# Performance work log

Measured on AMD Instinct MI355X. Metric: run time of the kernel, lower is better.

Reference implementation:

```python
import jax, jax.numpy as jnp
import numpy as np

EPS = 1e-4
TAU = 0.1
GAMMA = 64.0
RADIUS = 1.0
N_HEADS = 4
N_SPLIT = 4


def _l2norm(x, axis=-1):
    return x / jnp.maximum(jnp.linalg.norm(x, axis=axis, keepdims=True), 1e-12)


def _pd2(a, b):
    # pairwise squared distances: (B,N,M)
    return (jnp.sum(a * a, -1)[:, :, None] + jnp.sum(b * b, -1)[:, None, :]
            - 2.0 * jnp.einsum('bnd,bmd->bnm', a, b))


def _sim_matrix(xyz, nf, radius, gamma):
    # radius-masked Gaussian feature affinity, zero diagonal
    N = xyz.shape[1]
    d2x = _pd2(xyz, xyz)
    d2f = _pd2(nf, nf)
    A = jnp.exp(-gamma * d2f / nf.shape[-1]) * (d2x < radius * radius).astype(nf.dtype)
    return A * (1.0 - jnp.eye(N, dtype=A.dtype))


def _norm_lap(A, eps):
    deg = A.sum(-1)
    dinv = jax.lax.rsqrt(deg + eps)
    na = A * dinv[:, :, None] * dinv[:, None, :]
    lap = jnp.eye(A.shape[1], dtype=A.dtype) - na
    return lap, na


def _mincut(X, na, W1, b1, W2, b2, tau):
    # one GCN layer + temperature softmax soft assignment; pooled = weighted mean
    h = jax.nn.relu(jnp.einsum('bnm,bmc->bnc', na, X) @ W1 + b1)
    s = jax.nn.softmax((h @ W2 + b2) / tau, axis=-1)  # (B,N,K)
    denom = s.sum(1)[:, :, None] + EPS                # (B,K,1)
    c_fea = jnp.einsum('bnk,bnc->bkc', s, X) / denom
    return c_fea, s


def _centers(xyz, s):
    denom = s.sum(1)[:, :, None] + EPS
    return jnp.einsum('bnk,bnd->bkd', s, xyz) / denom


def _assignment_loss(p_xyz, c_xyz, s):
    d2 = _pd2(p_xyz, c_xyz)
    return jnp.mean(jnp.sum(s * d2, -1))


def _welsch(p_xyz, c_xyz, sigma):
    d2min = jnp.min(_pd2(p_xyz, c_xyz), -1)
    return jnp.mean(1.0 - jnp.exp(-d2min / (2.0 * sigma * sigma)))


def _knn_affinity(xyz, k):
    N = xyz.shape[1]
    d2 = _pd2(xyz, xyz)
    eye = jnp.eye(N, dtype=d2.dtype)
    neg = -(d2 + 1e6 * eye)
    thresh = jax.lax.top_k(neg, k)[0][..., -1:]
    mask = (neg >= thresh).astype(d2.dtype)
    A = jnp.exp(-d2) * mask * (1.0 - eye)
    return jnp.maximum(A, jnp.swapaxes(A, 1, 2))


def _cut_loss(na, xyz, alpha):
    N = xyz.shape[1]
    lap = jnp.eye(N, dtype=na.dtype) - na
    quad = jnp.einsum('bnd,bnm,bmd->b', xyz, lap, xyz)
    return alpha * jnp.mean(quad / N)


def _cross_attn(gf, cf, Wq, Wk, Wv, Wo, n_heads):
    B, N, C = gf.shape
    M = cf.shape[1]
    dh = C // n_heads
    q = (gf @ Wq).reshape(B, N, n_heads, dh)
    k = (cf @ Wk).reshape(B, M, n_heads, dh)
    v = (cf @ Wv).reshape(B, M, n_heads, dh)
    scores = jnp.einsum('bnhd,bmhd->bhnm', q, k) / np.sqrt(dh).astype(np.float32)
    attn = jax.nn.softmax(scores, -1)
    out = jnp.einsum('bhnm,bmhd->bnhd', attn, v).reshape(B, N, C) @ Wo
    return out, attn.mean(1)


def setup_inputs() -> dict:
    key = jax.random.key(0)
    ks = jax.random.split(key, 20)
    B, N_sp, C, H, K = 2, 1024, 256, 128, 64
    Kg = K // N_SPLIT
    sc = 1.0 / np.sqrt(C)
    sh = 1.0 / np.sqrt(H)
    return {
        'g_fea': jax.random.normal(ks[0], (B, N_sp, C), jnp.float32),
        'g_xyz': jax.random.uniform(ks[1], (B, N_sp, 3), jnp.float32),
        'p_fea_0': jax.random.normal(ks[2], (B, 4096, C), jnp.float32),
        'p_xyz_0': jax.random.uniform(ks[3], (B, 4096, 3), jnp.float32),
        'p_fea_1': jax.random.normal(ks[4], (B, 2048, C), jnp.float32),
        'p_xyz_1': jax.random.uniform(ks[5], (B, 2048, 3), jnp.float32),
        'lW1': jax.random.normal(ks[6], (C, H), jnp.float32) * sc,
        'lb1': jnp.zeros((H,), jnp.float32),
        'lW2': jax.random.normal(ks[7], (H, K), jnp.float32) * sh,
        'lb2': jnp.zeros((K,), jnp.float32),
        'gW1': jax.random.normal(ks[8], (C, H), jnp.float32) * sc,
        'gb1': jnp.zeros((H,), jnp.float32),
        'gW2': jax.random.normal(ks[9], (H, Kg), jnp.float32) * sh,
        'gb2': jnp.zeros((Kg,), jnp.float32),
        'Wq': jax.random.normal(ks[10], (C, C), jnp.float32) * sc,
        'Wk': jax.random.normal(ks[11], (C, C), jnp.float32) * sc,
        'Wv': jax.random.normal(ks[12], (C, C), jnp.float32) * sc,
        'Wo': jax.random.normal(ks[13], (C, C), jnp.float32) * sc,
    }


def reference(g_fea, g_xyz, p_fea_0, p_xyz_0, p_fea_1, p_xyz_1,
              lW1, lb1, lW2, lb2, gW1, gb1, gW2, gb2, Wq, Wk, Wv, Wo):
    l_loss = jnp.zeros((), jnp.float32)
    cx_list, cf_list = [], []
    for p_xyz_i, p_fea_i in ((p_xyz_0, p_fea_0), (p_xyz_1, p_fea_1)):
        nf = _l2norm(p_fea_i)
        A = _sim_matrix(p_xyz_i, nf, RADIUS, GAMMA)
        na = _norm_lap(A, EPS)[1]
        c_fea_i, s_i = _mincut(p_fea_i, na, lW1, lb1, lW2, lb2, TAU)
        c_xyz_i = _centers(p_xyz_i, s_i)
        c2p = jnp.einsum('bnk,bkc->bnc', s_i, jax.lax.stop_gradient(c_fea_i))
        l_loss = l_loss + _assignment_loss(p_xyz_i, c_xyz_i, s_i)
        l_loss = l_loss + jnp.linalg.norm(_l2norm(c2p) - nf) + _welsch(p_xyz_i, c_xyz_i, 1.0)
        cx_list.append(c_xyz_i)
        cf_list.append(c_fea_i)
    c_xyz = jnp.concatenate(cx_list, 1)
    c_fea = jnp.concatenate(cf_list, 1)
    A_c = _knn_affinity(c_xyz, 2 * N_SPLIT)
    na_c = _norm_lap(A_c, EPS)[1]
    c_fea_g, gs = _mincut(c_fea, na_c, gW1, gb1, gW2, gb2, TAU)
    c_xyz_g = _centers(c_xyz, gs)
    cut_loss_c = _assignment_loss(c_xyz, c_xyz_g, gs)
    agg, G_t = _cross_attn(g_fea, c_fea_g, Wq, Wk, Wv, Wo, N_HEADS)
    A_g = _sim_matrix(g_xyz, _l2norm(g_fea), 4.0 * RADIUS, GAMMA)
    ass_loss = _cut_loss(_norm_lap(A_g, EPS)[1], g_xyz, 1e-4)
    g_loss = jnp.mean(jnp.sum(jnp.linalg.norm(_l2norm(agg) - _l2norm(g_fea), axis=-1), 1)) + ass_loss
    return agg, l_loss + cut_loss_c, g_loss
```

## Files before the change

kernel.cpp:

```cpp
#include <hip/hip_runtime.h>

#define EPSF 1e-4f

typedef __attribute__((ext_vector_type(8))) short bf16x8;
typedef __attribute__((ext_vector_type(4))) float f32x4;

__device__ __forceinline__ unsigned short f2bf(float f){
    unsigned int u = __float_as_uint(f);
    return (unsigned short)((u + 0x7FFF + ((u >> 16) & 1)) >> 16);
}
__device__ __forceinline__ float bf2f(unsigned short u){
    return __uint_as_float(((unsigned int)u) << 16);
}
__device__ __forceinline__ float waveSum(float v){
    #pragma unroll
    for (int o = 32; o; o >>= 1) v += __shfl_xor(v, o, 64);
    return v;
}
__device__ __forceinline__ float waveMin(float v){
    #pragma unroll
    for (int o = 32; o; o >>= 1) v = fminf(v, __shfl_xor(v, o, 64));
    return v;
}
__device__ __forceinline__ float waveMax(float v){
// ... 5 lines not shown
    int t = threadIdx.x;
    red[t] = v; __syncthreads();
    for (int s = nthr >> 1; s > 0; s >>= 1){
        if (t < s) red[t] += red[t + s];
        __syncthreads();
    }
    float r = red[0]; __syncthreads();
    return r;
}

__global__ void l2norm_kernel(const float* __restrict__ x, float* __restrict__ outf,
                              unsigned short* __restrict__ outb, int rows){
    __shared__ float red[256];
    int row = blockIdx.x, t = threadIdx.x;
    float v = x[(long)row*256 + t];
    float s = blockReduceSum(v*v, red, 256);
    float nrm = fmaxf(sqrtf(s), 1e-12f);
    float r = v / nrm;
    outf[(long)row*256 + t] = r;
    outb[(long)row*256 + t] = f2bf(r);
}

__global__ void cvt_bf16_kernel(const float* __restrict__ in, unsigned short* __restrict__ out, long n4){
    long i = (long)blockIdx.x*256 + threadIdx.x;
    if (i < n4){
        float4 v = ((const float4*)in)[i];
        unsigned int lo = f2bf(v.x) | ((unsigned int)f2bf(v.y) << 16);
        unsigned int hi = f2bf(v.z) | ((unsigned int)f2bf(v.w) << 16);
        uint2 u; u.x = lo; u.y = hi;
        ((uint2*)out)[i] = u;
    }
}

__global__ void tcvt_kernel(const float* __restrict__ W, unsigned short* __restrict__ WT,
                            int Rw, int Cw){
    __shared__ float tile[64][65];
    int r0 = blockIdx.x*64, c0 = blockIdx.y*64;
    int t = threadIdx.x;
    for (int idx = t; idx < 4096; idx += 256){
        int rr = idx >> 6, cc = idx & 63;
        tile[rr][cc] = (r0+rr < Rw && c0+cc < Cw) ? W[(long)(r0+rr)*Cw + c0+cc] : 0.f;
    }
    __syncthreads();
    for (int idx = t; idx < 4096; idx += 256){
        int cc = idx >> 6, rr = idx & 63;
        if (r0+rr < Rw && c0+cc < Cw)
            WT[(long)(c0+cc)*Rw + r0+rr] = f2bf(tile[rr][cc]);
    }
}

__global__ __launch_bounds__(256) void gram_mfma_kernel(const unsigned short* __restrict__ nf,
                                                        const float* __restrict__ xyz,
                                                        unsigned short* __restrict__ A,
                                                        int N, float r2, float scale){
    __shared__ short tA[128*32], tB[128*32];
    __shared__ float xa[384], xb[384];
    int tid = threadIdx.x;
    int n0 = blockIdx.y*128, m0 = blockIdx.x*128;
    for (int i = tid; i < 384; i += 256){ xa[i] = xyz[n0*3 + i]; xb[i] = xyz[m0*3 + i]; }
    int w = tid >> 6, l = tid & 63;
    int wy = w >> 1, wx = w & 1;
    int lg = l >> 4, lr = l & 15;
    int srow = tid >> 2, sc = tid & 3;
    f32x4 zero = {0.f, 0.f, 0.f, 0.f};
    f32x4 acc[4][4];
    #pragma unroll
    for (int i = 0; i < 4; ++i)
        #pragma unroll
        for (int j = 0; j < 4; ++j) acc[i][j] = zero;
    for (int kt = 0; kt < 256; kt += 32){
        __syncthreads();
        #pragma unroll
        for (int p = 0; p < 2; ++p){
            int row = srow + p*64;
            uint4 va = *(const uint4*)(nf + (long)(n0+row)*256 + kt + sc*8);
            uint4 vb = *(const uint4*)(nf + (long)(m0+row)*256 + kt + sc*8);
            *(uint4*)(tA + row*32 + sc*8) = va;
            *(uint4*)(tB + row*32 + sc*8) = vb;
        }
        __syncthreads();
        bf16x8 af[4], bfr[4];
        #pragma unroll
        for (int f = 0; f < 4; ++f){
            af[f]  = *(const bf16x8*)(tA + (wy*64 + f*16 + lr)*32 + lg*8);
            bfr[f] = *(const bf16x8*)(tB + (wx*64 + f*16 + lr)*32 + lg*8);
        }
        #pragma unroll
        for (int i = 0; i < 4; ++i)
            #pragma unroll
            for (int j = 0; j < 4; ++j)
                acc[i][j] = __builtin_amdgcn_mfma_f32_16x16x32_bf16(af[i], bfr[j], acc[i][j], 0, 0, 0);
    }
    #pragma unroll
    for (int fi = 0; fi < 4; ++fi){
        #pragma unroll
        for (int fj = 0; fj < 4; ++fj){
            #pragma unroll
            for (int r = 0; r < 4; ++r){
                int n_ = wy*64 + fi*16 + lg*4 + r;
                int m_ = wx*64 + fj*16 + lr;
                float dx = xa[n_*3+0]-xb[m_*3+0];
                float dy = xa[n_*3+1]-xb[m_*3+1];
                float dz = xa[n_*3+2]-xb[m_*3+2];
                float d2x = dx*dx + dy*dy + dz*dz;
                int gn = n0 + n_, gm = m0 + m_;
                float dot = acc[fi][fj][r];
                float val = (d2x < r2 && gn != gm) ? expf(scale*(2.f*dot - 2.f)) : 0.f;
                A[(long)gn*N + gm] = f2bf(val);
            }
        }
    }
}

__global__ void rowsum_kernel(const unsigned short* __restrict__ A, float* __restrict__ dinv, int N){
    __shared__ float red[256];
    int n = blockIdx.x, t = threadIdx.x;
    const uint4* row = (const uint4*)(A + (long)n*N);
    float s = 0.f;
    for (int i = t; i < N/8; i += 256){
        uint4 u = row[i];
        s += __uint_as_float(u.x << 16) + __uint_as_float(u.x & 0xFFFF0000u);
        s += __uint_as_float(u.y << 16) + __uint_as_float(u.y & 0xFFFF0000u);
        s += __uint_as_float(u.z << 16) + __uint_as_float(u.z & 0xFFFF0000u);
        s += __uint_as_float(u.w << 16) + __uint_as_float(u.w & 0xFFFF0000u);
    }
    s = blockReduceSum(s, red, 256);
    if (t == 0) dinv[n] = rsqrtf(s + EPSF);
}

__global__ __launch_bounds__(256) void transpose_scale_kernel(const float* __restrict__ fea,
                                                              const float* __restrict__ dinv,
                                                              unsigned short* __restrict__ feaT,
                                                              unsigned short* __restrict__ xsT, int N){
    __shared__ float tile[64][65];
    __shared__ float dl[64];
    int m0 = blockIdx.x*64, c0 = blockIdx.y*64;
    int t = threadIdx.x;
    int lr = t >> 2, lc = (t & 3)*16;
    #pragma unroll
    for (int j = 0; j < 4; ++j){
        float4 v = *(const float4*)(fea + (long)(m0+lr)*256 + c0 + lc + j*4);
        tile[lr][lc+j*4+0] = v.x; tile[lr][lc+j*4+1] = v.y;
        tile[lr][lc+j*4+2] = v.z; tile[lr][lc+j*4+3] = v.w;
    }
    if (t < 64) dl[t] = dinv[m0+t];
    __syncthreads();
    unsigned short vr[16] __attribute__((aligned(16)));
    unsigned short vs[16] __attribute__((aligned(16)));
    #pragma unroll
    for (int j = 0; j < 16; ++j){
        float raw = tile[lc+j][lr];
        vr[j] = f2bf(raw);
        vs[j] = f2bf(raw * dl[lc+j]);
    }
    long off = (long)(c0+lr)*N + m0 + lc;
    *(uint4*)(feaT + off)     = *(uint4*)&vr[0];
    *(uint4*)(feaT + off + 8) = *(uint4*)&vr[8];
    *(uint4*)(xsT + off)      = *(uint4*)&vs[0];
    *(uint4*)(xsT + off + 8)  = *(uint4*)&vs[8];
}

__global__ __launch_bounds__(256) void ax_mfma_kernel(const unsigned short* __restrict__ A,
                                                      const unsigned short* __restrict__ xsT,
                                                      float* __restrict__ PY, int N){
    __shared__ short tA[128*32], tB[128*32];
    int tid = threadIdx.x;
    int c0 = blockIdx.x*128, n0 = blockIdx.y*128;
    int half = blockIdx.z;
    int kbase = half*(N/2), kend = kbase + N/2;
    int w = tid >> 6, l = tid & 63;
    int wy = w >> 1, wx = w & 1;
    int lg = l >> 4, lr = l & 15;
    int srow = tid >> 2, sc = tid & 3;
    f32x4 zero = {0.f, 0.f, 0.f, 0.f};
    f32x4 acc[4][4];
    #pragma unroll
    for (int i = 0; i < 4; ++i)
        #pragma unroll
        for (int j = 0; j < 4; ++j) acc[i][j] = zero;
    for (int kt = kbase; kt < kend; kt += 32){
        __syncthreads();
        #pragma unroll
        for (int p = 0; p < 2; ++p){
            int row = srow + p*64;
            uint4 va = *(const uint4*)(A   + (long)(n0+row)*N + kt + sc*8);
            uint4 vb = *(const uint4*)(xsT + (long)(c0+row)*N + kt + sc*8);
            *(uint4*)(tA + row*32 + sc*8) = va;
            *(uint4*)(tB + row*32 + sc*8) = vb;
        }
        __syncthreads();
        bf16x8 af[4], bfr[4];
        #pragma unroll
        for (int f = 0; f < 4; ++f){
            af[f]  = *(const bf16x8*)(tA + (wy*64 + f*16 + lr)*32 + lg*8);
            bfr[f] = *(const bf16x8*)(tB + (wx*64 + f*16 + lr)*32 + lg*8);
        }
        #pragma unroll
        for (int i = 0; i < 4; ++i)
            #pragma unroll
            for (int j = 0; j < 4; ++j)
                acc[i][j] = __builtin_amdgcn_mfma_f32_16x16x32_bf16(af[i], bfr[j], acc[i][j], 0, 0, 0);
    }
    float* out = PY + (long)half*N*256;
    #pragma unroll
    for (int fi = 0; fi < 4; ++fi){
        #pragma unroll
        for (int fj = 0; fj < 4; ++fj){
            #pragma unroll
            for (int r = 0; r < 4; ++r){
                int n_ = n0 + wy*64 + fi*16 + lg*4 + r;
                int c_ = c0 + wx*64 + fj*16 + lr;
                out[(long)n_*256 + c_] = acc[fi][fj][r];
            }
        }
    }
}

__global__ void combine_kernel(const float* __restrict__ PY, const float* __restrict__ dinv,
                               unsigned short* __restrict__ Yb, int N){
    long i = (long)blockIdx.x*256 + threadIdx.x;
    long e = i*8;
    const float4* p0 = (const float4*)(PY + e);
    const float4* p1 = (const float4*)(PY + (long)N*256 + e);
    float4 a0 = p0[0], a1 = p0[1], b0 = p1[0], b1 = p1[1];
    float d = dinv[e >> 8];
    unsigned short vb[8] __attribute__((aligned(16)));
    vb[0] = f2bf((a0.x+b0.x)*d); vb[1] = f2bf((a0.y+b0.y)*d);
    vb[2] = f2bf((a0.z+b0.z)*d); vb[3] = f2bf((a0.w+b0.w)*d);
    vb[4] = f2bf((a1.x+b1.x)*d); vb[5] = f2bf((a1.y+b1.y)*d);
    vb[6] = f2bf((a1.z+b1.z)*d); vb[7] = f2bf((a1.w+b1.w)*d);
    *(uint4*)(Yb + e) = *(uint4*)vb;
}

__global__ __launch_bounds__(256) void gemm_XW_mfma_kernel(const unsigned short* __restrict__ X,
                                                           const unsigned short* __restrict__ WT,
                                                           const float* __restrict__ bias,
                                                           float* __restrict__ outF,
                                                           unsigned short* __restrict__ outB,
                                                           int R, int Ci, int Co, int relu){
    __shared__ short tA[128*32], tB[128*32];
    int tid = threadIdx.x;
    int c0 = blockIdx.x*128, r0 = blockIdx.y*128;
    int w = tid >> 6, l = tid & 63;
    int wy = w >> 1, wx = w & 1;
    int lg = l >> 4, lr = l & 15;
    int srow = tid >> 2, sc = tid & 3;
    f32x4 zero = {0.f, 0.f, 0.f, 0.f};
    f32x4 acc[4][4];
    #pragma unroll
    for (int i = 0; i < 4; ++i)
        #pragma unroll
        for (int j = 0; j < 4; ++j) acc[i][j] = zero;
    for (int kt = 0; kt < Ci; kt += 32){
        __syncthreads();
        #pragma unroll
        for (int p = 0; p < 2; ++p){
            int row = srow + p*64;
            uint4 va = {0,0,0,0}, vb = {0,0,0,0};
            int ar = r0 + row, br = c0 + row;
            if (ar < R)  va = *(const uint4*)(X  + (long)ar*Ci + kt + sc*8);
            if (br < Co) vb = *(const uint4*)(WT + (long)br*Ci + kt + sc*8);
            *(uint4*)(tA + row*32 + sc*8) = va;
            *(uint4*)(tB + row*32 + sc*8) = vb;
        }
        __syncthreads();
        bf16x8 af[4], bfr[4];
        #pragma unroll
        for (int f = 0; f < 4; ++f){
            af[f]  = *(const bf16x8*)(tA + (wy*64 + f*16 + lr)*32 + lg*8);
            bfr[f] = *(const bf16x8*)(tB + (wx*64 + f*16 + lr)*32 + lg*8);
        }
        #pragma unroll
        for (int i = 0; i < 4; ++i)
            #pragma unroll
            for (int j = 0; j < 4; ++j)
                acc[i][j] = __builtin_amdgcn_mfma_f32_16x16x32_bf16(af[i], bfr[j], acc[i][j], 0, 0, 0);
    }
    #pragma unroll
    for (int fi = 0; fi < 4; ++fi){
        #pragma unroll
        for (int fj = 0; fj < 4; ++fj){
            #pragma unroll
            for (int r = 0; r < 4; ++r){
                int rr = r0 + wy*64 + fi*16 + lg*4 + r;
                int cc = c0 + wx*64 + fj*16 + lr;
                if (rr < R && cc < Co){
                    float v = acc[fi][fj][r] + (bias ? bias[cc] : 0.f);
                    if (relu) v = fmaxf(v, 0.f);
                    if (outF) outF[(long)rr*Co + cc] = v;
                    if (outB) outB[(long)rr*Co + cc] = f2bf(v);
                }
            }
        }
    }
}

__global__ __launch_bounds__(256) void softmaxT_kernel(float* __restrict__ s,
                                                       unsigned short* __restrict__ sT,
                                                       int sStride, float invtau){
    __shared__ unsigned short st[64][65];
    int blk = blockIdx.x, t = threadIdx.x, w = t >> 6, l = t & 63;
    #pragma unroll
    for (int i = 0; i < 16; ++i){
        int rloc = w + 4*i;
        long row = (long)blk*64 + rloc;
        float v = s[row*64 + l] * invtau;
        float mx = waveMax(v);
        float e = expf(v - mx);
        float sum = waveSum(e);
        float p = e / sum;
        s[row*64 + l] = p;
        st[l][rloc] = f2bf(p);
    }
    __syncthreads();
    int k = t >> 2, j = (t & 3)*16;
    unsigned short vbuf[16] __attribute__((aligned(16)));
    #pragma unroll
    for (int q = 0; q < 16; ++q) vbuf[q] = st[k][j+q];
    long off = (long)k*sStride + (long)blk*64 + j;
    *(uint4*)(sT + off)     = *(uint4*)&vbuf[0];
    *(uint4*)(sT + off + 8) = *(uint4*)&vbuf[8];
}

__global__ __launch_bounds__(256) void stx_mfma_kernel(const unsigned short* __restrict__ sT,
                                                       const unsigned short* __restrict__ feaT,
                                                       float* __restrict__ part,
                                                       int N, int split, int sStride){
    __shared__ short tA[64*32], tB[256*32];
    int tid = threadIdx.x;
    int z = blockIdx.x, b = z / split, chunk = z % split;
    int L = N / split, kst = chunk * L;
    const unsigned short* sTb = sT + (long)b*N;
    const unsigned short* fT  = feaT + (long)b*256*N;
    int w = tid >> 6, l = tid & 63;
    int lg = l >> 4, lr = l & 15;
    f32x4 zero = {0.f, 0.f, 0.f, 0.f};
    f32x4 acc[4][4];
    #pragma unroll
    for (int i = 0; i < 4; ++i)
        #pragma unroll
        for (int j = 0; j < 4; ++j) acc[i][j] = zero;
    int srow = tid >> 2, koff = (tid & 3)*8;
    for (int kt = kst; kt < kst + L; kt += 32){
        __syncthreads();
        *(uint4*)(tA + srow*32 + koff) = *(const uint4*)(sTb + (long)srow*sStride + kt + koff);
        #pragma unroll
        for (int p = 0; p < 4; ++p){
            int row = srow + p*64;
            *(uint4*)(tB + row*32 + koff) = *(const uint4*)(fT + (long)row*N + kt + koff);
        }
        __syncthreads();
        bf16x8 af[4], bfr[4];
        #pragma unroll
        for (int f = 0; f < 4; ++f){
            af[f]  = *(const bf16x8*)(tA + (f*16 + lr)*32 + lg*8);
            bfr[f] = *(const bf16x8*)(tB + (w*64 + f*16 + lr)*32 + lg*8);
        }
        #pragma unroll
        for (int i = 0; i < 4; ++i)
            #pragma unroll
            for (int j = 0; j < 4; ++j)
                acc[i][j] = __builtin_amdgcn_mfma_f32_16x16x32_bf16(af[i], bfr[j], acc[i][j], 0, 0, 0);
    }
    float* outp = part + (long)z*64*256;
    #pragma unroll
    for (int fi = 0; fi < 4; ++fi){
        #pragma unroll
        for (int fj = 0; fj < 4; ++fj){
            #pragma unroll
            for (int r = 0; r < 4; ++r){
                int kc = fi*16 + lg*4 + r;
                int cc = w*64 + fj*16 + lr;
                outp[(long)kc*256 + cc] = acc[fi][fj][r];
            }
        }
    }
}

__global__ __launch_bounds__(256) void gemm_XW_kernel(const float* __restrict__ X,
                                                      const float* __restrict__ W,
                                                      const float* __restrict__ bias,
                                                      float* __restrict__ out,
                                                      int R, int Ci, int Co, int relu){
    __shared__ float sa[32][65], sb[32][65];
    int tid = threadIdx.x, tx = tid & 15, ty = tid >> 4;
    int c0 = blockIdx.x * 64, r0 = blockIdx.y * 64;
    float acc[4][4] = {};
    for (int kt = 0; kt < Ci; kt += 32){
        #pragma unroll
        for (int p = 0; p < 8; ++p){
            int idx = p*256 + tid;
            int k = idx & 31, i = idx >> 5;
            int rr = r0 + i;
            sa[k][i] = (rr < R) ? X[(long)rr*Ci + kt + k] : 0.f;
            int j = idx & 63, kk = idx >> 6;
            int cc = c0 + j;
            sb[kk][j] = (cc < Co) ? W[(long)(kt+kk)*Co + cc] : 0.f;
        }
        __syncthreads();
        #pragma unroll
        for (int k = 0; k < 32; ++k){
            float a0=sa[k][ty*4+0],a1=sa[k][ty*4+1],a2=sa[k][ty*4+2],a3=sa[k][ty*4+3];
            float b0=sb[k][tx*4+0],b1=sb[k][tx*4+1],b2=sb[k][tx*4+2],b3=sb[k][tx*4+3];
            acc[0][0]+=a0*b0; acc[0][1]+=a0*b1; acc[0][2]+=a0*b2; acc[0][3]+=a0*b3;
            acc[1][0]+=a1*b0; acc[1][1]+=a1*b1; acc[1][2]+=a1*b2; acc[1][3]+=a1*b3;
            acc[2][0]+=a2*b0; acc[2][1]+=a2*b1; acc[2][2]+=a2*b2; acc[2][3]+=a2*b3;
            acc[3][0]+=a3*b0; acc[3][1]+=a3*b1; acc[3][2]+=a3*b2; acc[3][3]+=a3*b3;
        }
        __syncthreads();
    }
    #pragma unroll
    for (int r = 0; r < 4; ++r){
        #pragma unroll
        for (int c = 0; c < 4; ++c){
            int rr = r0 + ty*4 + r, cc = c0 + tx*4 + c;
            if (rr < R && cc < Co){
                float v = acc[r][c] + (bias ? bias[cc] : 0.f);
                if (relu) v = fmaxf(v, 0.f);
                out[(long)rr*Co + cc] = v;
            }
        }
    }
}

__global__ void softmax_kernel(float* __restrict__ x, int Kc, float tau){
    int row = blockIdx.x, lane = threadIdx.x;
    bool act = lane < Kc;
    float v = act ? x[(long)row*Kc + lane] / tau : -1e30f;
    float mx = v;
    #pragma unroll
    for (int o = 32; o; o >>= 1) mx = fmaxf(mx, __shfl_xor(mx, o, 64));
    float e = act ? expf(v - mx) : 0.f;
    float s = e;
    #pragma unroll
    for (int o = 32; o; o >>= 1) s += __shfl_xor(s, o, 64);
    if (act) x[(long)row*Kc + lane] = e / s;
}

__global__ void cluster_xyz_kernel(const float* __restrict__ s, const float* __restrict__ xyz,
                                   float* __restrict__ outx, float* __restrict__ outd,
                                   int N, int Kc, int xBS, int dBS){
    __shared__ float red[256];
    int b = blockIdx.y, k = blockIdx.x, t = threadIdx.x;
    s   += (long)b*N*Kc;
    xyz += (long)b*N*3;
    float a0=0,a1=0,a2=0,ad=0;
    for (int n = t; n < N; n += 256){
        float sv = s[(long)n*Kc + k];
        ad += sv;
        a0 += sv*xyz[n*3+0]; a1 += sv*xyz[n*3+1]; a2 += sv*xyz[n*3+2];
    }
    a0 = blockReduceSum(a0, red, 256);
    a1 = blockReduceSum(a1, red, 256);
    a2 = blockReduceSum(a2, red, 256);
    ad = blockReduceSum(ad, red, 256);
    if (t == 0){
        outx[b*xBS + k*3+0] = a0;
        outx[b*xBS + k*3+1] = a1;
        outx[b*xBS + k*3+2] = a2;
        outd[b*dBS + k] = ad;
    }
}

__global__ __launch_bounds__(256) void gemm_sTX_kernel(const float* __restrict__ s,
                                                       const float* __restrict__ X,
                                                       float* __restrict__ part,
                                                       int N, int Kc, int split,
                                                       long sBS, long xBS){
    __shared__ float sa[32][65], sb[32][65];
    int tid = threadIdx.x, tx = tid & 15, ty = tid >> 4;
    int c0 = blockIdx.x * 64;
    int b = blockIdx.z / split, chunk = blockIdx.z % split;
// ... 153 lines not shown

__global__ void cutc_kernel(const float* __restrict__ gs, const float* __restrict__ cxyz,
                            const float* __restrict__ cxyzg, float* __restrict__ scal, float inv){
    __shared__ float cg[48];
    __shared__ float red[128];
    int b = blockIdx.x, t = threadIdx.x;
    if (t < 48) cg[t] = cxyzg[b*48 + t];
    __syncthreads();
    float x0 = cxyz[b*384 + t*3+0], x1 = cxyz[b*384 + t*3+1], x2 = cxyz[b*384 + t*3+2];
    float acc = 0.f;
    #pragma unroll
    for (int k = 0; k < 16; ++k){
        float dx = x0-cg[k*3+0], dy = x1-cg[k*3+1], dz = x2-cg[k*3+2];
        acc += gs[b*2048 + t*16 + k]*(dx*dx+dy*dy+dz*dz);
    }
    acc = blockReduceSum(acc, red, 128);
    if (t == 0) atomicAdd(&scal[b], acc*inv);
}

__global__ __launch_bounds__(256) void attn_kernel(const float* __restrict__ q,
                                                   const float* __restrict__ kk,
                                                   const float* __restrict__ vv,
                                                   unsigned short* __restrict__ aob){
    __shared__ float Ks[16][256], Vs[16][256];
    int b = blockIdx.y, n = blockIdx.x, t = threadIdx.x;
    #pragma unroll
    for (int p = 0; p < 16; ++p){
        int j = p*256 + t;
        Ks[j>>8][j&255] = kk[b*4096 + j];
        Vs[j>>8][j&255] = vv[b*4096 + j];
    }
    __syncthreads();
    float qv = q[((long)b*1024 + n)*256 + t];
    float sc[16];
    #pragma unroll
    for (int m = 0; m < 16; ++m){
        float v = qv * Ks[m][t];
        #pragma unroll
        for (int o = 32; o; o >>= 1) v += __shfl_xor(v, o, 64);
        sc[m] = v * 0.125f;
    }
    float mx = -1e30f;
    #pragma unroll
    for (int m = 0; m < 16; ++m) mx = fmaxf(mx, sc[m]);
    float sum = 0.f;
    #pragma unroll
    for (int m = 0; m < 16; ++m){ sc[m] = expf(sc[m]-mx); sum += sc[m]; }
    float o = 0.f;
    #pragma unroll
    for (int m = 0; m < 16; ++m) o += sc[m]*Vs[m][t];
    aob[((long)b*1024 + n)*256 + t] = f2bf(o / sum);
}

__global__ void quad_kernel(const unsigned short* __restrict__ A, const float* __restrict__ dinv,
                            const float* __restrict__ xyz, float* __restrict__ scal){
    __shared__ float part[4];
    int t = threadIdx.x, w = t >> 6, l = t & 63;
    int n = blockIdx.x*4 + w;
    float a0=0,a1=0,a2=0;
    #pragma unroll 4
    for (int i = 0; i < 16; ++i){
        int m = l + i*64;
        float wv = bf2f(A[(long)n*1024 + m])*dinv[m];
        a0 += wv*xyz[m*3+0]; a1 += wv*xyz[m*3+1]; a2 += wv*xyz[m*3+2];
    }
    a0 = waveSum(a0); a1 = waveSum(a1); a2 = waveSum(a2);
    if (l == 0){
        float x0 = xyz[n*3+0], x1 = xyz[n*3+1], x2 = xyz[n*3+2];
        part[w] = (x0*x0+x1*x1+x2*x2) - dinv[n]*(x0*a0+x1*a1+x2*a2);
    }
    __syncthreads();
    if (t == 0) atomicAdd(&scal[4*64 + (blockIdx.x & 63)], part[0]+part[1]+part[2]+part[3]);
}

__global__ void gloss_kernel(const float* __restrict__ agg, const float* __restrict__ gfea,
                             float* __restrict__ scal){
    __shared__ float part[4];
    int t = threadIdx.x, w = t >> 6, l = t & 63;
    long r = (long)blockIdx.x*4 + w;
    const float* a = agg + r*256;
    const float* g = gfea + r*256;
    float a0=a[l],a1=a[l+64],a2=a[l+128],a3=a[l+192];
    float g0=g[l],g1=g[l+64],g2=g[l+128],g3=g[l+192];
    float na2 = waveSum(a0*a0+a1*a1+a2*a2+a3*a3);
    float ng2 = waveSum(g0*g0+g1*g1+g2*g2+g3*g3);
    float ia = 1.f/fmaxf(sqrtf(na2), 1e-12f), ig = 1.f/fmaxf(sqrtf(ng2), 1e-12f);
    float e0=a0*ia-g0*ig, e1=a1*ia-g1*ig, e2=a2*ia-g2*ig, e3=a3*ia-g3*ig;
    float d2 = waveSum(e0*e0+e1*e1+e2*e2+e3*e3);
    if (l == 0) part[w] = sqrtf(d2);
    __syncthreads();
    if (t == 0) atomicAdd(&scal[3*64 + (blockIdx.x & 63)], part[0]+part[1]+part[2]+part[3]);
}

__global__ void finalize_kernel(const float* __restrict__ scal, float* __restrict__ out){
    int t = threadIdx.x;
    float s[5];
    #pragma unroll
    for (int q = 0; q < 5; ++q){
        float v = scal[q*64 + t];
        #pragma unroll
        for (int o = 32; o; o >>= 1) v += __shfl_xor(v, o, 64);
        s[q] = v;
    }
    if (t == 0){
        out[524288] = s[0] + sqrtf(s[1]) + sqrtf(s[2]);
        out[524289] = s[3]*0.5f + 1e-4f*s[4]/2048.0f;
    }
}

extern "C" void kernel_launch(void* const* d_in, const int* in_sizes, int n_in,
                              void* d_out, int out_size, void* d_ws, size_t ws_size,
                              hipStream_t stream){
    const float* g_fea   = (const float*)d_in[0];
    const float* g_xyz   = (const float*)d_in[1];
    const float* p_fea_0 = (const float*)d_in[2];
    const float* p_xyz_0 = (const float*)d_in[3];
    const float* p_fea_1 = (const float*)d_in[4];
    const float* p_xyz_1 = (const float*)d_in[5];
    const float* lW1 = (const float*)d_in[6];
    const float* lb1 = (const float*)d_in[7];
    const float* lW2 = (const float*)d_in[8];
    const float* lb2 = (const float*)d_in[9];
    const float* gW1 = (const float*)d_in[10];
    const float* gb1 = (const float*)d_in[11];
    const float* gW2 = (const float*)d_in[12];
    const float* gb2 = (const float*)d_in[13];
    const float* Wq = (const float*)d_in[14];
    const float* Wk = (const float*)d_in[15];
    const float* Wv = (const float*)d_in[16];
    const float* Wo = (const float*)d_in[17];
    float* out = (float*)d_out;
    float* ws_f = (float*)d_ws;

    constexpr long O_SCALS = 0;
    constexpr long O_CFEA  = 512;
    constexpr long O_CXYZ  = O_CFEA + 65536;
    constexpr long O_DEN   = O_CXYZ + 768;
    constexpr long O_CFG   = O_DEN  + 256;
    constexpr long O_CXG   = O_CFG  + 8192;
    constexpr long O_DENG  = O_CXG  + 96;
    constexpr long O_PART  = O_DENG + 64;
    constexpr long O_NF    = O_PART + 262144;
    constexpr long O_NFB   = O_NF   + 2097152;
    constexpr long O_XST   = O_NFB  + 1048576;
    constexpr long O_FEAT  = O_XST  + 1048576;
    constexpr long O_YB    = O_FEAT + 1048576;
    constexpr long O_HB    = O_YB   + 1048576;
    constexpr long O_S     = O_HB   + 524288;
    constexpr long O_ST    = O_S    + 524288;
    constexpr long O_DINV  = O_ST   + 262144;
    constexpr long O_PY    = O_DINV + 8192;
    constexpr long O_A     = O_PY   + 2097152;
    constexpr long O_Q     = O_A    + 8388608;
    constexpr long O_GFB   = O_Q    + 524288;
    constexpr long O_AOB   = O_GFB  + 262144;
    constexpr long O_KK    = O_AOB  + 262144;
    constexpr long O_VV    = O_KK   + 8192;
    constexpr long O_NAC   = O_VV   + 8192;
    constexpr long O_Y2    = O_NAC  + 32768;
    constexpr long O_H2    = O_Y2   + 65536;
    constexpr long O_LG2   = O_H2   + 32768;
    constexpr long O_W1T   = O_LG2  + 4096;
    constexpr long O_W2T   = O_W1T  + 16384;
    constexpr long O_WQT   = O_W2T  + 4096;
    constexpr long O_WOT   = O_WQT  + 32768;

    hipMemsetAsync(ws_f + O_SCALS, 0, 512*sizeof(float), stream);

    float* nf   = ws_f + O_NF;
    unsigned short* nfb  = (unsigned short*)(ws_f + O_NFB);
    unsigned short* xsT  = (unsigned short*)(ws_f + O_XST);
    unsigned short* feaT = (unsigned short*)(ws_f + O_FEAT);
    unsigned short* Ybb  = (unsigned short*)(ws_f + O_YB);
    unsigned short* Hb   = (unsigned short*)(ws_f + O_HB);
    unsigned short* sTb  = (unsigned short*)(ws_f + O_ST);
    unsigned short* A    = (unsigned short*)(ws_f + O_A);
    unsigned short* gfb  = (unsigned short*)(ws_f + O_GFB);
    unsigned short* aob  = (unsigned short*)(ws_f + O_AOB);
    unsigned short* lW1T = (unsigned short*)(ws_f + O_W1T);
    unsigned short* lW2T = (unsigned short*)(ws_f + O_W2T);
    unsigned short* WqT  = (unsigned short*)(ws_f + O_WQT);
    unsigned short* WoT  = (unsigned short*)(ws_f + O_WOT);
    float* sb   = ws_f + O_S;
    float* dinv = ws_f + O_DINV;
    float* PY   = ws_f + O_PY;
    float* part = ws_f + O_PART;
    float* Qf   = ws_f + O_Q;

    tcvt_kernel<<<dim3(4, 2), 256, 0, stream>>>(lW1, lW1T, 256, 128);
    tcvt_kernel<<<dim3(2, 1), 256, 0, stream>>>(lW2, lW2T, 128, 64);
    tcvt_kernel<<<dim3(4, 4), 256, 0, stream>>>(Wq, WqT, 256, 256);
    tcvt_kernel<<<dim3(4, 4), 256, 0, stream>>>(Wo, WoT, 256, 256);
    cvt_bf16_kernel<<<512, 256, 0, stream>>>(g_fea, gfb, 131072);

    struct Lvl { const float* fea; const float* xyz; int N; int k0; int ndsSlot; };
    Lvl lv[2] = {{p_fea_0, p_xyz_0, 4096, 0, 1}, {p_fea_1, p_xyz_1, 2048, 64, 2}};

    for (int L = 0; L < 2; ++L){
        int N = lv[L].N;
        const float* fea = lv[L].fea;
        const float* xyz = lv[L].xyz;
        l2norm_kernel<<<2*N, 256, 0, stream>>>(fea, nf, nfb, 2*N);
        for (int b = 0; b < 2; ++b){
            const unsigned short* nfbb = nfb + (long)b*N*256;
            const float* xyzb = xyz + (long)b*N*3;
            gram_mfma_kernel<<<dim3(N/128, N/128), 256, 0, stream>>>(nfbb, xyzb, A, N, 1.0f, 0.25f);
            rowsum_kernel<<<N, 256, 0, stream>>>(A, dinv + b*N, N);
            transpose_scale_kernel<<<dim3(N/64, 4), 256, 0, stream>>>(fea + (long)b*N*256, dinv + b*N,
                                                                      feaT + (long)b*256*N,
                                                                      xsT + (long)b*256*N, N);
            ax_mfma_kernel<<<dim3(2, N/128, 2), 256, 0, stream>>>(A, xsT + (long)b*256*N, PY, N);
            combine_kernel<<<N/8, 256, 0, stream>>>(PY, dinv + b*N, Ybb + (long)b*N*256, N);
        }
        gemm_XW_mfma_kernel<<<dim3(1, 2*N/128), 256, 0, stream>>>(Ybb, lW1T, lb1, nullptr, Hb,
                                                                  2*N, 256, 128, 1);
        gemm_XW_mfma_kernel<<<dim3(1, 2*N/128), 256, 0, stream>>>(Hb, lW2T, lb2, sb, nullptr,
                                                                  2*N, 128, 64, 0);
        softmaxT_kernel<<<2*N/64, 256, 0, stream>>>(sb, sTb, 2*N, 10.0f);
        cluster_xyz_kernel<<<dim3(64, 2), 256, 0, stream>>>(sb, xyz, ws_f + O_CXYZ + lv[L].k0*3,
                                                            ws_f + O_DEN + lv[L].k0, N, 64, 384, 128);
        stx_mfma_kernel<<<16, 256, 0, stream>>>(sTb, feaT, part, N, 8, 2*N);
        divide_sum_kernel<<<dim3(64, 2), 256, 0, stream>>>(part, ws_f + O_DEN + lv[L].k0,
                                                           ws_f + O_CFEA + lv[L].k0*256,
                                                           ws_f + O_CXYZ + lv[L].k0*3,
                                                           64, 8, 128*256, 384, 128);
        level_loss_kernel<<<dim3(N/4, 2), 256, 0, stream>>>(sb, xyz, ws_f + O_CXYZ + lv[L].k0*3,
                                                            ws_f + O_CFEA + lv[L].k0*256, nf,
                                                            ws_f + O_SCALS, N, 1.0f/(2.0f*N), lv[L].ndsSlot);
    }

    knn_nac_kernel<<<2, 128, 0, stream>>>(ws_f + O_CXYZ, ws_f + O_NAC);
    bmm_small_kernel<<<dim3(128, 2), 256, 0, stream>>>(ws_f + O_NAC, ws_f + O_CFEA, ws_f + O_Y2);
    gemm_XW_kernel<<<dim3(2, 4), 256, 0, stream>>>(ws_f + O_Y2, gW1, gb1, ws_f + O_H2, 256, 256, 128, 1);
    gemm_XW_kernel<<<dim3(1, 4), 256, 0, stream>>>(ws_f + O_H2, gW2, gb2, ws_f + O_LG2, 256, 128, 16, 0);
    softmax_kernel<<<256, 64, 0, stream>>>(ws_f + O_LG2, 16, 0.1f);
    cluster_xyz_kernel<<<dim3(16, 2), 256, 0, stream>>>(ws_f + O_LG2, ws_f + O_CXYZ,
                                                        ws_f + O_CXG, ws_f + O_DENG, 128, 16, 48, 16);
    gemm_sTX_kernel<<<dim3(4, 1, 2), 256, 0, stream>>>(ws_f + O_LG2, ws_f + O_CFEA, part,
                                                       128, 16, 1, 128L*16, 128L*256);
    divide_sum_kernel<<<dim3(16, 2), 256, 0, stream>>>(part, ws_f + O_DENG, ws_f + O_CFG,
                                                       ws_f + O_CXG, 16, 1, 16*256, 48, 16);
    cutc_kernel<<<2, 128, 0, stream>>>(ws_f + O_LG2, ws_f + O_CXYZ, ws_f + O_CXG,
                                       ws_f + O_SCALS, 1.0f/256.0f);

    gemm_XW_mfma_kernel<<<dim3(2, 16), 256, 0, stream>>>(gfb, WqT, nullptr, Qf, nullptr,
                                                         2048, 256, 256, 0);
    gemm_XW_kernel<<<dim3(4, 1), 256, 0, stream>>>(ws_f + O_CFG, Wk, nullptr, ws_f + O_KK, 32, 256, 256, 0);
    gemm_XW_kernel<<<dim3(4, 1), 256, 0, stream>>>(ws_f + O_CFG, Wv, nullptr, ws_f + O_VV, 32, 256, 256, 0);
    attn_kernel<<<dim3(1024, 2), 256, 0, stream>>>(Qf, ws_f + O_KK, ws_f + O_VV, aob);
    gemm_XW_mfma_kernel<<<dim3(2, 16), 256, 0, stream>>>(aob, WoT, nullptr, out, nullptr,
                                                         2048, 256, 256, 0);

    l2norm_kernel<<<2048, 256, 0, stream>>>(g_fea, nf, nfb, 2048);
    for (int b = 0; b < 2; ++b){
        gram_mfma_kernel<<<dim3(8, 8), 256, 0, stream>>>(nfb + (long)b*1024*256, g_xyz + (long)b*1024*3,
                                                         A, 1024, 16.0f, 0.25f);
        rowsum_kernel<<<1024, 256, 0, stream>>>(A, dinv + b*1024, 1024);
        quad_kernel<<<256, 256, 0, stream>>>(A, dinv + b*1024, g_xyz + (long)b*1024*3, ws_f + O_SCALS);
    }

    gloss_kernel<<<512, 256, 0, stream>>>(out, g_fea, ws_f + O_SCALS);
    finalize_kernel<<<1, 64, 0, stream>>>(ws_f + O_SCALS, out);
}
```

Measured before the change: 906.8 us.

## Fuse degree rowsum into gram epilogue and split-K the small GEMMs

The gram kernel now accumulates each row's affinity sum in its epilogue, reduces it across lanes, and atomically adds it into a zeroed degree buffer. This removes the separate rowsum kernel, which re-read the whole bf16 affinity matrix, and consumers compute rsqrt(deg+eps) themselves. The small FP32 GEMMs on the global level and for K/V are replaced by a split-K kernel plus a combine kernel, and the stx and sTX reductions use more splits, to raise parallelism on tiny problems. The cost is atomics, extra combine launches, a larger workspace memset, and degrees summed in fp32 before bf16 rounding, which differs slightly from summing the rounded bf16 values.

```diff
diff --git a/kernel.cpp b/kernel.cpp
--- a/kernel.cpp
+++ b/kernel.cpp
@@ -81,6 +81,7 @@
 __global__ __launch_bounds__(256) void gram_mfma_kernel(const unsigned short* __restrict__ nf,
                                                         const float* __restrict__ xyz,
                                                         unsigned short* __restrict__ A,
+                                                        float* __restrict__ deg,
                                                         int N, float r2, float scale){
     __shared__ short tA[128*32], tB[128*32];
     __shared__ float xa[384], xb[384];
@@ -123,42 +124,34 @@
     #pragma unroll
     for (int fi = 0; fi < 4; ++fi){
         #pragma unroll
-        for (int fj = 0; fj < 4; ++fj){
+        for (int r = 0; r < 4; ++r){
+            int n_ = wy*64 + fi*16 + lg*4 + r;
+            int gn = n0 + n_;
+            float rowacc = 0.f;
             #pragma unroll
-            for (int r = 0; r < 4; ++r){
-                int n_ = wy*64 + fi*16 + lg*4 + r;
+            for (int fj = 0; fj < 4; ++fj){
                 int m_ = wx*64 + fj*16 + lr;
                 float dx = xa[n_*3+0]-xb[m_*3+0];
                 float dy = xa[n_*3+1]-xb[m_*3+1];
                 float dz = xa[n_*3+2]-xb[m_*3+2];
                 float d2x = dx*dx + dy*dy + dz*dz;
-                int gn = n0 + n_, gm = m0 + m_;
+                int gm = m0 + m_;
                 float dot = acc[fi][fj][r];
                 float val = (d2x < r2 && gn != gm) ? expf(scale*(2.f*dot - 2.f)) : 0.f;
                 A[(long)gn*N + gm] = f2bf(val);
+                rowacc += val;
             }
-        }
-    }
-}
-
-__global__ void rowsum_kernel(const unsigned short* __restrict__ A, float* __restrict__ dinv, int N){
-    __shared__ float red[256];
-    int n = blockIdx.x, t = threadIdx.x;
-    const uint4* row = (const uint4*)(A + (long)n*N);
-    float s = 0.f;
-    for (int i = t; i < N/8; i += 256){
-        uint4 u = row[i];
-        s += __uint_as_float(u.x << 16) + __uint_as_float(u.x & 0xFFFF0000u);
-        s += __uint_as_float(u.y << 16) + __uint_as_float(u.y & 0xFFFF0000u);
-        s += __uint_as_float(u.z << 16) + __uint_as_float(u.z & 0xFFFF0000u);
-        s += __uint_as_float(u.w << 16) + __uint_as_float(u.w & 0xFFFF0000u);
-    }
-    s = blockReduceSum(s, red, 256);
-    if (t == 0) dinv[n] = rsqrtf(s + EPSF);
+            rowacc += __shfl_xor(rowacc, 1, 64);
+            rowacc += __shfl_xor(rowacc, 2, 64);
+            rowacc += __shfl_xor(rowacc, 4, 64);
+            rowacc += __shfl_xor(rowacc, 8, 64);
+            if (lr == 0) atomicAdd(&deg[gn], rowacc);
+        }
+    }
 }
 
 __global__ __launch_bounds__(256) void transpose_scale_kernel(const float* __restrict__ fea,
-                                                              const float* __restrict__ dinv,
+                                                              const float* __restrict__ deg,
                                                               unsigned short* __restrict__ feaT,
                                                               unsigned short* __restrict__ xsT, int N){
     __shared__ float tile[64][65];
@@ -172,7 +165,7 @@
         tile[lr][lc+j*4+0] = v.x; tile[lr][lc+j*4+1] = v.y;
         tile[lr][lc+j*4+2] = v.z; tile[lr][lc+j*4+3] = v.w;
     }
-    if (t < 64) dl[t] = dinv[m0+t];
+    if (t < 64) dl[t] = rsqrtf(deg[m0+t] + EPSF);
     __syncthreads();
     unsigned short vr[16] __attribute__((aligned(16)));
     unsigned short vs[16] __attribute__((aligned(16)));
@@ -245,14 +238,14 @@
     }
 }
 
-__global__ void combine_kernel(const float* __restrict__ PY, const float* __restrict__ dinv,
+__global__ void combine_kernel(const float* __restrict__ PY, const float* __restrict__ deg,
                                unsigned short* __restrict__ Yb, int N){
     long i = (long)blockIdx.x*256 + threadIdx.x;
     long e = i*8;
     const float4* p0 = (const float4*)(PY + e);
     const float4* p1 = (const float4*)(PY + (long)N*256 + e);
     float4 a0 = p0[0], a1 = p0[1], b0 = p1[0], b1 = p1[1];
-    float d = dinv[e >> 8];
+    float d = rsqrtf(deg[e >> 8] + EPSF);
     unsigned short vb[8] __attribute__((aligned(16)));
     vb[0] = f2bf((a0.x+b0.x)*d); vb[1] = f2bf((a0.y+b0.y)*d);
     vb[2] = f2bf((a0.z+b0.z)*d); vb[3] = f2bf((a0.w+b0.w)*d);
@@ -324,6 +317,65 @@
     }
 }
 
+__global__ __launch_bounds__(256) void gemm_splitk_kernel(const float* __restrict__ X,
+                                                          const float* __restrict__ W0,
+                                                          const float* __restrict__ W1,
+                                                          float* __restrict__ part,
+                                                          int R, int Ci, int Co, int Ks){
+    __shared__ float sa[32][65], sb[32][65];
+    int tid = threadIdx.x, tx = tid & 15, ty = tid >> 4;
+    int c0 = blockIdx.x * 64, r0 = blockIdx.y * 64;
+    int z = blockIdx.z;
+    const float* W = (z / Ks) ? W1 : W0;
+    int kchunk = Ci / Ks, kst = (z % Ks) * kchunk;
+    float acc[4][4] = {};
+    for (int kt = kst; kt < kst + kchunk; kt += 32){
+        #pragma unroll
+        for (int p = 0; p < 8; ++p){
+            int idx = p*256 + tid;
+            int k = idx & 31, i = idx >> 5;
+            int rr = r0 + i;
+            sa[k][i] = (rr < R) ? X[(long)rr*Ci + kt + k] : 0.f;
+            int j = idx & 63, kk = idx >> 6;
+            int cc = c0 + j;
+            sb[kk][j] = (cc < Co) ? W[(long)(kt+kk)*Co + cc] : 0.f;
+        }
+        __syncthreads();
+        #pragma unroll
+        for (int k = 0; k < 32; ++k){
+            float a0=sa[k][ty*4+0],a1=sa[k][ty*4+1],a2=sa[k][ty*4+2],a3=sa[k][ty*4+3];
+            float b0=sb[k][tx*4+0],b1=sb[k][tx*4+1],b2=sb[k][tx*4+2],b3=sb[k][tx*4+3];
+            acc[0][0]+=a0*b0; acc[0][1]+=a0*b1; acc[0][2]+=a0*b2; acc[0][3]+=a0*b3;
+            acc[1][0]+=a1*b0; acc[1][1]+=a1*b1; acc[1][2]+=a1*b2; acc[1][3]+=a1*b3;
+            acc[2][0]+=a2*b0; acc[2][1]+=a2*b1; acc[2][2]+=a2*b2; acc[2][3]+=a2*b3;
+            acc[3][0]+=a3*b0; acc[3][1]+=a3*b1; acc[3][2]+=a3*b2; acc[3][3]+=a3*b3;
+        }
+        __syncthreads();
+    }
+    float* outp = part + (long)z*R*Co;
+    #pragma unroll
+    for (int r = 0; r < 4; ++r){
+        #pragma unroll
+        for (int c = 0; c < 4; ++c){
+            int rr = r0 + ty*4 + r, cc = c0 + tx*4 + c;
+            if (rr < R && cc < Co) outp[(long)rr*Co + cc] = acc[r][c];
+        }
+    }
+}
+
+__global__ void combine_bias_kernel(const float* __restrict__ part, const float* __restrict__ bias,
+                                    float* __restrict__ out, int R, int Co, int Ks, int relu){
+    long i = (long)blockIdx.x*256 + threadIdx.x;
+    if (i < (long)R*Co){
+        long zs = (long)R*Co;
+        float s = 0.f;
+        for (int q = 0; q < Ks; ++q) s += part[q*zs + i];
+        float v = s + (bias ? bias[i % Co] : 0.f);
+        if (relu) v = fmaxf(v, 0.f);
+        out[i] = v;
+    }
+}
+
 __global__ __launch_bounds__(256) void softmaxT_kernel(float* __restrict__ s,
                                                        unsigned short* __restrict__ sT,
                                                        int sStride, float invtau){
@@ -401,52 +453,6 @@
                 int kc = fi*16 + lg*4 + r;
                 int cc = w*64 + fj*16 + lr;
                 outp[(long)kc*256 + cc] = acc[fi][fj][r];
-            }
-        }
-    }
-}
-
-__global__ __launch_bounds__(256) void gemm_XW_kernel(const float* __restrict__ X,
-                                                      const float* __restrict__ W,
-                                                      const float* __restrict__ bias,
-                                                      float* __restrict__ out,
-                                                      int R, int Ci, int Co, int relu){
-    __shared__ float sa[32][65], sb[32][65];
-    int tid = threadIdx.x, tx = tid & 15, ty = tid >> 4;
-    int c0 = blockIdx.x * 64, r0 = blockIdx.y * 64;
-    float acc[4][4] = {};
-    for (int kt = 0; kt < Ci; kt += 32){
-        #pragma unroll
-        for (int p = 0; p < 8; ++p){
-            int idx = p*256 + tid;
-            int k = idx & 31, i = idx >> 5;
-            int rr = r0 + i;
-            sa[k][i] = (rr < R) ? X[(long)rr*Ci + kt + k] : 0.f;
-            int j = idx & 63, kk = idx >> 6;
-            int cc = c0 + j;
-            sb[kk][j] = (cc < Co) ? W[(long)(kt+kk)*Co + cc] : 0.f;
-        }
-        __syncthreads();
-        #pragma unroll
-        for (int k = 0; k < 32; ++k){
-            float a0=sa[k][ty*4+0],a1=sa[k][ty*4+1],a2=sa[k][ty*4+2],a3=sa[k][ty*4+3];
-            float b0=sb[k][tx*4+0],b1=sb[k][tx*4+1],b2=sb[k][tx*4+2],b3=sb[k][tx*4+3];
-            acc[0][0]+=a0*b0; acc[0][1]+=a0*b1; acc[0][2]+=a0*b2; acc[0][3]+=a0*b3;
-            acc[1][0]+=a1*b0; acc[1][1]+=a1*b1; acc[1][2]+=a1*b2; acc[1][3]+=a1*b3;
-            acc[2][0]+=a2*b0; acc[2][1]+=a2*b1; acc[2][2]+=a2*b2; acc[2][3]+=a2*b3;
-            acc[3][0]+=a3*b0; acc[3][1]+=a3*b1; acc[3][2]+=a3*b2; acc[3][3]+=a3*b3;
-        }
-        __syncthreads();
-    }
-    #pragma unroll
-    for (int r = 0; r < 4; ++r){
-        #pragma unroll
-        for (int c = 0; c < 4; ++c){
-            int rr = r0 + ty*4 + r, cc = c0 + tx*4 + c;
-            if (rr < R && cc < Co){
-                float v = acc[r][c] + (bias ? bias[cc] : 0.f);
-                if (relu) v = fmaxf(v, 0.f);
-                out[(long)rr*Co + cc] = v;
             }
         }
     }
@@ -706,7 +712,7 @@
     aob[((long)b*1024 + n)*256 + t] = f2bf(o / sum);
 }
 
-__global__ void quad_kernel(const unsigned short* __restrict__ A, const float* __restrict__ dinv,
+__global__ void quad_kernel(const unsigned short* __restrict__ A, const float* __restrict__ deg,
                             const float* __restrict__ xyz, float* __restrict__ scal){
     __shared__ float part[4];
     int t = threadIdx.x, w = t >> 6, l = t & 63;
@@ -715,13 +721,14 @@
     #pragma unroll 4
     for (int i = 0; i < 16; ++i){
         int m = l + i*64;
-        float wv = bf2f(A[(long)n*1024 + m])*dinv[m];
+        float wv = bf2f(A[(long)n*1024 + m])*rsqrtf(deg[m] + EPSF);
         a0 += wv*xyz[m*3+0]; a1 += wv*xyz[m*3+1]; a2 += wv*xyz[m*3+2];
     }
     a0 = waveSum(a0); a1 = waveSum(a1); a2 = waveSum(a2);
     if (l == 0){
         float x0 = xyz[n*3+0], x1 = xyz[n*3+1], x2 = xyz[n*3+2];
-        part[w] = (x0*x0+x1*x1+x2*x2) - dinv[n]*(x0*a0+x1*a1+x2*a2);
+        float dn = rsqrtf(deg[n] + EPSF);
+        part[w] = (x0*x0+x1*x1+x2*x2) - dn*(x0*a0+x1*a1+x2*a2);
     }
     __syncthreads();
     if (t == 0) atomicAdd(&scal[4*64 + (blockIdx.x & 63)], part[0]+part[1]+part[2]+part[3]);
@@ -787,14 +794,15 @@
     float* ws_f = (float*)d_ws;
 
     constexpr long O_SCALS = 0;
-    constexpr long O_CFEA  = 512;
+    constexpr long O_DEG   = O_SCALS + 512;
+    constexpr long O_CFEA  = 16384;
     constexpr long O_CXYZ  = O_CFEA + 65536;
     constexpr long O_DEN   = O_CXYZ + 768;
     constexpr long O_CFG   = O_DEN  + 256;
     constexpr long O_CXG   = O_CFG  + 8192;
     constexpr long O_DENG  = O_CXG  + 96;
     constexpr long O_PART  = O_DENG + 64;
-    constexpr long O_NF    = O_PART + 262144;
+    constexpr long O_NF    = O_PART + 524288;
     constexpr long O_NFB   = O_NF   + 2097152;
     constexpr long O_XST   = O_NFB  + 1048576;
     constexpr long O_FEAT  = O_XST  + 1048576;
@@ -802,8 +810,7 @@
     constexpr long O_HB    = O_YB   + 1048576;
     constexpr long O_S     = O_HB   + 524288;
     constexpr long O_ST    = O_S    + 524288;
-    constexpr long O_DINV  = O_ST   + 262144;
-    constexpr long O_PY    = O_DINV + 8192;
+    constexpr long O_PY    = O_ST   + 262144;
     constexpr long O_A     = O_PY   + 2097152;
     constexpr long O_Q     = O_A    + 8388608;
     constexpr long O_GFB   = O_Q    + 524288;
@@ -819,7 +826,7 @@
     constexpr long O_WQT   = O_W2T  + 4096;
     constexpr long O_WOT   = O_WQT  + 32768;
 
-    hipMemsetAsync(ws_f + O_SCALS, 0, 512*sizeof(float), stream);
+    hipMemsetAsync(ws_f + O_SCALS, 0, (512 + 14336)*sizeof(float), stream);
 
     float* nf   = ws_f + O_NF;
     unsigned short* nfb  = (unsigned short*)(ws_f + O_NFB);
@@ -836,7 +843,7 @@
     unsigned short* WqT  = (unsigned short*)(ws_f + O_WQT);
     unsigned short* WoT  = (unsigned short*)(ws_f + O_WOT);
     float* sb   = ws_f + O_S;
-    float* dinv = ws_f + O_DINV;
+    float* degA = ws_f + O_DEG;
     float* PY   = ws_f + O_PY;
     float* part = ws_f + O_PART;
     float* Qf   = ws_f + O_Q;
@@ -847,8 +854,8 @@
     tcvt_kernel<<<dim3(4, 4), 256, 0, stream>>>(Wo, WoT, 256, 256);
     cvt_bf16_kernel<<<512, 256, 0, stream>>>(g_fea, gfb, 131072);
 
-    struct Lvl { const float* fea; const float* xyz; int N; int k0; int ndsSlot; };
-    Lvl lv[2] = {{p_fea_0, p_xyz_0, 4096, 0, 1}, {p_fea_1, p_xyz_1, 2048, 64, 2}};
+    struct Lvl { const float* fea; const float* xyz; int N; int k0; int ndsSlot; long degBase; };
+    Lvl lv[2] = {{p_fea_0, p_xyz_0, 4096, 0, 1, 0}, {p_fea_1, p_xyz_1, 2048, 64, 2, 8192}};
 
     for (int L = 0; L < 2; ++L){
         int N = lv[L].N;
@@ -856,15 +863,15 @@
         const float* xyz = lv[L].xyz;
         l2norm_kernel<<<2*N, 256, 0, stream>>>(fea, nf, nfb, 2*N);
         for (int b = 0; b < 2; ++b){
-            const unsigned short* nfbb = nfb + (long)b*N*256;
-            const float* xyzb = xyz + (long)b*N*3;
-            gram_mfma_kernel<<<dim3(N/128, N/128), 256, 0, stream>>>(nfbb, xyzb, A, N, 1.0f, 0.25f);
-            rowsum_kernel<<<N, 256, 0, stream>>>(A, dinv + b*N, N);
-            transpose_scale_kernel<<<dim3(N/64, 4), 256, 0, stream>>>(fea + (long)b*N*256, dinv + b*N,
+            float* degb = degA + lv[L].degBase + (long)b*N;
+            gram_mfma_kernel<<<dim3(N/128, N/128), 256, 0, stream>>>(nfb + (long)b*N*256,
+                                                                     xyz + (long)b*N*3, A, degb,
+                                                                     N, 1.0f, 0.25f);
+            transpose_scale_kernel<<<dim3(N/64, 4), 256, 0, stream>>>(fea + (long)b*N*256, degb,
                                                                       feaT + (long)b*256*N,
                                                                       xsT + (long)b*256*N, N);
             ax_mfma_kernel<<<dim3(2, N/128, 2), 256, 0, stream>>>(A, xsT + (long)b*256*N, PY, N);
-            combine_kernel<<<N/8, 256, 0, stream>>>(PY, dinv + b*N, Ybb + (long)b*N*256, N);
+            combine_kernel<<<N/8, 256, 0, stream>>>(PY, degb, Ybb + (long)b*N*256, N);
         }
         gemm_XW_mfma_kernel<<<dim3(1, 2*N/128), 256, 0, stream>>>(Ybb, lW1T, lb1, nullptr, Hb,
                                                                   2*N, 256, 128, 1);
@@ -873,11 +880,11 @@
         softmaxT_kernel<<<2*N/64, 256, 0, stream>>>(sb, sTb, 2*N, 10.0f);
         cluster_xyz_kernel<<<dim3(64, 2), 256, 0, stream>>>(sb, xyz, ws_f + O_CXYZ + lv[L].k0*3,
                                                             ws_f + O_DEN + lv[L].k0, N, 64, 384, 128);
-        stx_mfma_kernel<<<16, 256, 0, stream>>>(sTb, feaT, part, N, 8, 2*N);
+        stx_mfma_kernel<<<32, 256, 0, stream>>>(sTb, feaT, part, N, 16, 2*N);
         divide_sum_kernel<<<dim3(64, 2), 256, 0, stream>>>(part, ws_f + O_DEN + lv[L].k0,
                                                            ws_f + O_CFEA + lv[L].k0*256,
                                                            ws_f + O_CXYZ + lv[L].k0*3,
-                                                           64, 8, 128*256, 384, 128);
+                                                           64, 16, 128*256, 384, 128);
         level_loss_kernel<<<dim3(N/4, 2), 256, 0, stream>>>(sb, xyz, ws_f + O_CXYZ + lv[L].k0*3,
                                                             ws_f + O_CFEA + lv[L].k0*256, nf,
                                                             ws_f + O_SCALS, N, 1.0f/(2.0f*N), lv[L].ndsSlot);
@@ -885,32 +892,38 @@
 
     knn_nac_kernel<<<2, 128, 0, stream>>>(ws_f + O_CXYZ, ws_f + O_NAC);
     bmm_small_kernel<<<dim3(128, 2), 256, 0, stream>>>(ws_f + O_NAC, ws_f + O_CFEA, ws_f + O_Y2);
-    gemm_XW_kernel<<<dim3(2, 4), 256, 0, stream>>>(ws_f + O_Y2, gW1, gb1, ws_f + O_H2, 256, 256, 128, 1);
-    gemm_XW_kernel<<<dim3(1, 4), 256, 0, stream>>>(ws_f + O_H2, gW2, gb2, ws_f + O_LG2, 256, 128, 16, 0);
+    gemm_splitk_kernel<<<dim3(2, 4, 4), 256, 0, stream>>>(ws_f + O_Y2, gW1, nullptr, part,
+                                                          256, 256, 128, 4);
+    combine_bias_kernel<<<128, 256, 0, stream>>>(part, gb1, ws_f + O_H2, 256, 128, 4, 1);
+    gemm_splitk_kernel<<<dim3(1, 4, 4), 256, 0, stream>>>(ws_f + O_H2, gW2, nullptr, part,
+                                                          256, 128, 16, 4);
+    combine_bias_kernel<<<16, 256, 0, stream>>>(part, gb2, ws_f + O_LG2, 256, 16, 4, 0);
     softmax_kernel<<<256, 64, 0, stream>>>(ws_f + O_LG2, 16, 0.1f);
     cluster_xyz_kernel<<<dim3(16, 2), 256, 0, stream>>>(ws_f + O_LG2, ws_f + O_CXYZ,
                                                         ws_f + O_CXG, ws_f + O_DENG, 128, 16, 48, 16);
-    gemm_sTX_kernel<<<dim3(4, 1, 2), 256, 0, stream>>>(ws_f + O_LG2, ws_f + O_CFEA, part,
-                                                       128, 16, 1, 128L*16, 128L*256);
+    gemm_sTX_kernel<<<dim3(4, 1, 8), 256, 0, stream>>>(ws_f + O_LG2, ws_f + O_CFEA, part,
+                                                       128, 16, 4, 128L*16, 128L*256);
     divide_sum_kernel<<<dim3(16, 2), 256, 0, stream>>>(part, ws_f + O_DENG, ws_f + O_CFG,
-                                                       ws_f + O_CXG, 16, 1, 16*256, 48, 16);
+                                                       ws_f + O_CXG, 16, 4, 16*256, 48, 16);
     cutc_kernel<<<2, 128, 0, stream>>>(ws_f + O_LG2, ws_f + O_CXYZ, ws_f + O_CXG,
                                        ws_f + O_SCALS, 1.0f/256.0f);
 
     gemm_XW_mfma_kernel<<<dim3(2, 16), 256, 0, stream>>>(gfb, WqT, nullptr, Qf, nullptr,
                                                          2048, 256, 256, 0);
-    gemm_XW_kernel<<<dim3(4, 1), 256, 0, stream>>>(ws_f + O_CFG, Wk, nullptr, ws_f + O_KK, 32, 256, 256, 0);
-    gemm_XW_kernel<<<dim3(4, 1), 256, 0, stream>>>(ws_f + O_CFG, Wv, nullptr, ws_f + O_VV, 32, 256, 256, 0);
+    gemm_splitk_kernel<<<dim3(4, 1, 16), 256, 0, stream>>>(ws_f + O_CFG, Wk, Wv, part,
+                                                           32, 256, 256, 8);
+    combine_bias_kernel<<<32, 256, 0, stream>>>(part, nullptr, ws_f + O_KK, 32, 256, 8, 0);
+    combine_bias_kernel<<<32, 256, 0, stream>>>(part + 8L*32*256, nullptr, ws_f + O_VV, 32, 256, 8, 0);
     attn_kernel<<<dim3(1024, 2), 256, 0, stream>>>(Qf, ws_f + O_KK, ws_f + O_VV, aob);
     gemm_XW_mfma_kernel<<<dim3(2, 16), 256, 0, stream>>>(aob, WoT, nullptr, out, nullptr,
                                                          2048, 256, 256, 0);
 
     l2norm_kernel<<<2048, 256, 0, stream>>>(g_fea, nf, nfb, 2048);
     for (int b = 0; b < 2; ++b){
+        float* degb = degA + 12288 + (long)b*1024;
         gram_mfma_kernel<<<dim3(8, 8), 256, 0, stream>>>(nfb + (long)b*1024*256, g_xyz + (long)b*1024*3,
-                                                         A, 1024, 16.0f, 0.25f);
-        rowsum_kernel<<<1024, 256, 0, stream>>>(A, dinv + b*1024, 1024);
-        quad_kernel<<<256, 256, 0, stream>>>(A, dinv + b*1024, g_xyz + (long)b*1024*3, ws_f + O_SCALS);
+                                                         A, degb, 1024, 16.0f, 0.25f);
+        quad_kernel<<<256, 256, 0, stream>>>(A, degb, g_xyz + (long)b*1024*3, ws_f + O_SCALS);
     }
 
     gloss_kernel<<<512, 256, 0, stream>>>(out, g_fea, ws_f + O_SCALS);
```

Measured after the change: 782.9 us. -13.7%, faster.
